# Performance work log

Measured on AMD Instinct MI355X. Metric: run time of the kernel, lower is better.

## Reference

```python
import jax, jax.numpy as jnp
import numpy as np

COEF = 0.99 - 1.0  # module stores coef - 1


def setup_inputs() -> dict:
    key = jax.random.key(0)
    B = 32768
    steps = 4096
    x = jax.random.normal(key, (B, 1), dtype=jnp.float32)
    delta_t = 0.01  # python float, as in the torch signature
    return {"steps": steps, "x": x, "delta_t": delta_t}


def reference(steps, x, delta_t):
    # Recurrence out[t] = out[t-1] * (1 + COEF*delta_t), out[0] = x[:,0]
    # Closed form: out[:, t] = x[:, 0] * r**t  (geometric decay)
    r = jnp.asarray(1.0 + COEF * delta_t, dtype=x.dtype)
    t = jnp.arange(steps, dtype=x.dtype)           # (steps,)
    out = x[:, 0:1] * jnp.power(r, t)[None, :]      # (B, steps)
    return out[:, :, None]                          # (B, steps, 1)
```

## Files before the change

### kernel.cpp

```cpp
#include <hip/hip_runtime.h>


__global__ __launch_bounds__(256) void air_res_vec4(
    const float* __restrict__ x,
    const float* __restrict__ dt_p,
    float4* __restrict__ out,
    int B, int steps4)
{
    const long long tid      = (long long)blockIdx.x * blockDim.x + threadIdx.x;
    const long long nthreads = (long long)gridDim.x * blockDim.x;

    int b        = (int)(tid / steps4);
    const int tq = (int)(tid % steps4);
    const int bstep = (int)(nthreads / steps4);

    const double COEF = 0.99 - 1.0;
    const double rd   = 1.0 + COEF * (double)dt_p[0];
    const float  rf   = (float)rd;
    const float  p    = (float)exp2((double)(4 * tq) * log2(rd));

    for (; b < B; b += bstep) {
        const float v0 = x[b] * p;
        const float v1 = v0 * rf;
        const float v2 = v1 * rf;
        const float v3 = v2 * rf;
        out[(long long)b * steps4 + tq] = make_float4(v0, v1, v2, v3);
    }
}

__global__ __launch_bounds__(256) void air_res_scalar(
    const float* __restrict__ x,
    const float* __restrict__ dt_p,
    float* __restrict__ out,
    int B, int steps)
{
    const long long total    = (long long)B * steps;
    const long long nthreads = (long long)gridDim.x * blockDim.x;
    const double COEF = 0.99 - 1.0;
    const double rd   = 1.0 + COEF * (double)dt_p[0];
    const double l2r  = log2(rd);

    for (long long i = (long long)blockIdx.x * blockDim.x + threadIdx.x;
         i < total; i += nthreads) {
        const int b = (int)(i / steps);
        const int t = (int)(i % steps);
        out[i] = x[b] * (float)exp2((double)t * l2r);
    }
}

extern "C" void kernel_launch(void* const* d_in, const int* in_sizes, int n_in,
                              void* d_out, int out_size, void* d_ws, size_t ws_size,
                              hipStream_t stream) {
    const float* x    = (const float*)d_in[1];
    const float* dt_p = (const float*)d_in[2];
    float* out        = (float*)d_out;

    const int B     = in_sizes[1];
    const int steps = out_size / B;

    const int threads = 256;
    const int blocks  = 2048;

    const long long nthreads = (long long)blocks * threads;
    if ((steps % 4) == 0 && (nthreads % (steps / 4)) == 0) {
        air_res_vec4<<<blocks, threads, 0, stream>>>(
            x, dt_p, (float4*)out, B, steps / 4);
    } else {
        air_res_scalar<<<blocks, threads, 0, stream>>>(x, dt_p, out, B, steps);
    }
}
```

Before: 111.6 us.

## Assign contiguous rows per wavefront and stream powers with a running multiplier

The work split changes from one thread per float4 column across all rows to one wavefront per block of contiguous rows. Each wave writes whole rows as 1 KB float4 chunks, advancing by a precomputed r^256 multiplier instead of a per-thread power. The grid shrinks from 2048 to 256 blocks, so each wave streams 32 full rows. This aims for longer sequential write streams, but with only 1024 waves in flight the kernel may not keep enough stores outstanding to saturate HBM, and the running product accumulates some float rounding error.

After: 107.5 us. -3.7%, faster.

```diff
diff --git a/kernel.cpp b/kernel.cpp
--- a/kernel.cpp
+++ b/kernel.cpp
@@ -1,30 +1,41 @@
 #include <hip/hip_runtime.h>
 
 
-__global__ __launch_bounds__(256) void air_res_vec4(
+typedef float vfloat4 __attribute__((ext_vector_type(4)));
+
+__global__ __launch_bounds__(256) void air_res_stream(
     const float* __restrict__ x,
     const float* __restrict__ dt_p,
-    float4* __restrict__ out,
-    int B, int steps4)
+    float* __restrict__ out,
+    int B, int steps, int rpw)
 {
-    const long long tid      = (long long)blockIdx.x * blockDim.x + threadIdx.x;
-    const long long nthreads = (long long)gridDim.x * blockDim.x;
-
-    int b        = (int)(tid / steps4);
-    const int tq = (int)(tid % steps4);
-    const int bstep = (int)(nthreads / steps4);
+    const int lane = threadIdx.x & 63;
+    const int wv   = threadIdx.x >> 6;
+    const int wpb  = blockDim.x >> 6;
+    const long long gw = (long long)blockIdx.x * wpb + wv;
 
     const double COEF = 0.99 - 1.0;
     const double rd   = 1.0 + COEF * (double)dt_p[0];
+    const double l2r  = log2(rd);
     const float  rf   = (float)rd;
-    const float  p    = (float)exp2((double)(4 * tq) * log2(rd));
+    const float  r2   = (float)(rd * rd);
+    const float  r3   = (float)(rd * rd * rd);
+    const float  s_lane = (float)exp2((double)(4 * lane) * l2r);
+    const float  rstep  = (float)exp2((double)256.0 * l2r);
+    const int    iters  = steps >> 8;
 
-    for (; b < B; b += bstep) {
-        const float v0 = x[b] * p;
-        const float v1 = v0 * rf;
-        const float v2 = v1 * rf;
-        const float v3 = v2 * rf;
-        out[(long long)b * steps4 + tq] = make_float4(v0, v1, v2, v3);
+    int row = (int)(gw * rpw);
+    const int row_end = row + rpw;
+    for (; row < row_end; ++row) {
+        const float xb = x[row];
+        float xs = xb * s_lane;
+        float* p = out + (long long)row * steps + 4 * lane;
+#pragma unroll 4
+        for (int i = 0; i < iters; ++i) {
+            *(vfloat4*)p = (vfloat4){xs, xs * rf, xs * r2, xs * r3};
+            xs *= rstep;
+            p  += 256;
+        }
     }
 }
 
@@ -59,13 +70,13 @@
     const int steps = out_size / B;
 
     const int threads = 256;
-    const int blocks  = 2048;
+    const int blocks  = 256;
+    const int nwaves  = blocks * (threads / 64);
 
-    const long long nthreads = (long long)blocks * threads;
-    if ((steps % 4) == 0 && (nthreads % (steps / 4)) == 0) {
-        air_res_vec4<<<blocks, threads, 0, stream>>>(
-            x, dt_p, (float4*)out, B, steps / 4);
+    if ((steps % 256) == 0 && (B % nwaves) == 0) {
+        air_res_stream<<<blocks, threads, 0, stream>>>(
+            x, dt_p, out, B, steps, B / nwaves);
     } else {
-        air_res_scalar<<<blocks, threads, 0, stream>>>(x, dt_p, out, B, steps);
+        air_res_scalar<<<2048, threads, 0, stream>>>(x, dt_p, out, B, steps);
     }
 }
```
